# Performance work log

Measured on AMD Instinct MI355X. Metric: run time of the kernel, lower is better.

Reference implementation:

```python
import jax, jax.numpy as jnp
import numpy as np
from jax import lax

DN = ('NCHW', 'OIHW', 'NCHW')

def dsconv(x, dw_w, dw_b, pw_w, pw_b, dilation):
    # depthwise 3x3 (groups = C), padding = dilation, then pointwise 1x1
    C = x.shape[1]
    y = lax.conv_general_dilated(
        x, dw_w, window_strides=(1, 1),
        padding=[(dilation, dilation), (dilation, dilation)],
        rhs_dilation=(dilation, dilation),
        dimension_numbers=DN, feature_group_count=C)
    y = y + dw_b[None, :, None, None]
    y = lax.conv_general_dilated(y, pw_w, window_strides=(1, 1), padding='VALID',
                                 dimension_numbers=DN)
    return y + pw_b[None, :, None, None]


def setup_inputs() -> dict:
    key = jax.random.key(0)
    ks = jax.random.split(key, 16)
    B, C, H, W = 4, 256, 64, 64
    R = C // 8  # reduced_channels = 32
    s = 0.05
    inp = {
        'x': jax.random.normal(ks[0], (B, C, H, W), dtype=jnp.float32),
        # conv1 (dilation 1)
        'c1_dw_w': jax.random.normal(ks[1], (C, 1, 3, 3), dtype=jnp.float32) * s,
        'c1_dw_b': jax.random.normal(ks[2], (C,), dtype=jnp.float32) * s,
        'c1_pw_w': jax.random.normal(ks[3], (R, C, 1, 1), dtype=jnp.float32) * s,
        'c1_pw_b': jax.random.normal(ks[4], (R,), dtype=jnp.float32) * s,
        # conv2 (dilation 3)
        'c2_dw_w': jax.random.normal(ks[5], (C, 1, 3, 3), dtype=jnp.float32) * s,
        'c2_dw_b': jax.random.normal(ks[6], (C,), dtype=jnp.float32) * s,
        'c2_pw_w': jax.random.normal(ks[7], (R, C, 1, 1), dtype=jnp.float32) * s,
        'c2_pw_b': jax.random.normal(ks[8], (R,), dtype=jnp.float32) * s,
        # conv3 (dilation 5)
        'c3_dw_w': jax.random.normal(ks[9], (C, 1, 3, 3), dtype=jnp.float32) * s,
        'c3_dw_b': jax.random.normal(ks[10], (C,), dtype=jnp.float32) * s,
        'c3_pw_w': jax.random.normal(ks[11], (R, C, 1, 1), dtype=jnp.float32) * s,
        'c3_pw_b': jax.random.normal(ks[12], (R,), dtype=jnp.float32) * s,
        # conv_out 1x1: R -> C
        'co_w': jax.random.normal(ks[13], (C, R, 1, 1), dtype=jnp.float32) * s,
        'co_b': jax.random.normal(ks[14], (C,), dtype=jnp.float32) * s,
    }
    return inp


def reference(x, c1_dw_w, c1_dw_b, c1_pw_w, c1_pw_b,
              c2_dw_w, c2_dw_b, c2_pw_w, c2_pw_b,
              c3_dw_w, c3_dw_b, c3_pw_w, c3_pw_b,
              co_w, co_b):
    B, C, H, W = x.shape
    R = C // 8
    N = H * W
    Fp1 = dsconv(x, c1_dw_w, c1_dw_b, c1_pw_w, c1_pw_b, 1).reshape(B, R, N)
    Fp2 = dsconv(x, c2_dw_w, c2_dw_b, c2_pw_w, c2_pw_b, 3).reshape(B, R, N)
    Fp3 = dsconv(x, c3_dw_w, c3_dw_b, c3_pw_w, c3_pw_b, 5).reshape(B, R, N)
    # Mpam[b,i,j] = sum_c Fp2[b,c,i] * Fp3[b,c,j]; softmax over j
    Mpam = jax.nn.softmax(jnp.einsum('bci,bcj->bij', Fp2, Fp3), axis=-1)
    # Fpmap[b,c,i] = sum_j Fp1[b,c,j] * Mpam[i,j]  (matmul with Mpam^T)
    Fpmap = jnp.einsum('bcj,bij->bci', Fp1, Mpam).reshape(B, R, H, W)
    Fpmap = lax.conv_general_dilated(Fpmap, co_w, (1, 1), 'VALID',
                                     dimension_numbers=DN) + co_b[None, :, None, None]
    return x + Fpmap
```

## Files before the change

### kernel.cpp

```cpp
#include <hip/hip_runtime.h>
#include <stdint.h>

#define BB 4
#define CC 256
#define NN 4096
#define RR 32
#define NCHUNK 8
#define JSTEPS (NN / NCHUNK / 32)
#define CSIZE  (NN / NCHUNK)

typedef __attribute__((ext_vector_type(8)))  short  short8;
typedef __attribute__((ext_vector_type(4)))  short  short4v;
typedef __attribute__((ext_vector_type(16))) float  floatx16;

#if defined(__has_builtin)
#if __has_builtin(__builtin_amdgcn_cvt_pk_bf16_f32)
#define HAVE_PK_BF16 1
#endif
#endif

#ifdef HAVE_PK_BF16
typedef __attribute__((ext_vector_type(2))) __bf16 bf16x2;
#endif

static __device__ __forceinline__ unsigned short f2bf_sw(float f) {
    union { float f; unsigned int u; } v; v.f = f;
    unsigned int u = v.u;
    u += 0x7fffu + ((u >> 16) & 1u);
    return (unsigned short)(u >> 16);
}

static __device__ __forceinline__ unsigned int pk_bf16(float a, float b) {
#ifdef HAVE_PK_BF16
    bf16x2 r = __builtin_amdgcn_cvt_pk_bf16_f32(a, b);
    unsigned int u; __builtin_memcpy(&u, &r, 4); return u;
#else
    return (unsigned int)f2bf_sw(a) | ((unsigned int)f2bf_sw(b) << 16);
#endif
}

static __device__ __forceinline__ unsigned short f2bf(float f) {
#ifdef HAVE_PK_BF16
    return (unsigned short)(pk_bf16(f, 0.f) & 0xffffu);
#else
    return f2bf_sw(f);
#endif
}

static __device__ __forceinline__ float bf2f(unsigned short u) {
    union { unsigned int u; float f; } v; v.u = ((unsigned int)u) << 16;
    return v.f;
}

static __device__ __forceinline__ float exp2_fast(float x) {
#if __has_builtin(__builtin_amdgcn_exp2f)
    return __builtin_amdgcn_exp2f(x);
#else
    return exp2f(x);
#endif
}

__global__ __launch_bounds__(256, 4) void k_dw(
    const float* __restrict__ x,
    const float* __restrict__ w1, const float* __restrict__ b1,
    const float* __restrict__ w2, const float* __restrict__ b2,
    const float* __restrict__ w3, const float* __restrict__ b3,
    unsigned short* __restrict__ Dq)
{
    int t = threadIdx.x, lane = t & 63, wv = t >> 6;
    int c = blockIdx.x, b = blockIdx.y;
    int hb = wv * 16;
    const float* xc = x + ((size_t)(b * CC + c)) * NN;
    float row[26];
    #pragma unroll
    for (int k = 0; k < 26; k++) {
        int rr = hb - 5 + k;
        int rc = rr < 0 ? 0 : (rr > 63 ? 63 : rr);
        float v = xc[rc * 64 + lane];
        row[k] = (rr >= 0 && rr <= 63) ? v : 0.f;
    }
    const float* DWW[3] = {w1, w2, w3};
    const float* DWB[3] = {b1, b2, b3};
    #pragma unroll
    for (int p = 0; p < 3; p++) {
        const int d = (p == 0) ? 1 : (p == 1 ? 3 : 5);
        float wt[9];
        #pragma unroll
        for (int q = 0; q < 9; q++) wt[q] = DWW[p][c * 9 + q];
        float bias = DWB[p][c];
        bool okl = lane >= d, okr = lane < 64 - d;
        int lml = okl ? lane - d : 0;
        int lpr = okr ? lane + d : 63;
        float sm[26], sp[26];
        #pragma unroll
        for (int k = 5 - d; k <= 20 + d; k++) {
            float a = __shfl(row[k], lml, 64); sm[k] = okl ? a : 0.f;
            float q2 = __shfl(row[k], lpr, 64); sp[k] = okr ? q2 : 0.f;
        }
        unsigned short* Dp = Dq + (((size_t)p * BB + b) * CC + c) * NN;
        #pragma unroll
        for (int hl = 0; hl < 16; hl++) {
            int k0 = hl + 5 - d, k1 = hl + 5, k2 = hl + 5 + d;
            float o = bias
                + wt[0] * sm[k0] + wt[1] * row[k0] + wt[2] * sp[k0]
                + wt[3] * sm[k1] + wt[4] * row[k1] + wt[5] * sp[k1]
                + wt[6] * sm[k2] + wt[7] * row[k2] + wt[8] * sp[k2];
            Dp[(hb + hl) * 64 + lane] = f2bf(o);
        }
    }
}

__global__ __launch_bounds__(256, 2) void k_pw(
    const unsigned short* __restrict__ Dq,
    const float* __restrict__ p1, const float* __restrict__ pb1,
    const float* __restrict__ p2, const float* __restrict__ pb2,
    const float* __restrict__ p3, const float* __restrict__ pb3,
    unsigned short* __restrict__ V, unsigned short* __restrict__ Qt,
    unsigned short* __restrict__ Kt)
{
    __shared__ unsigned short PW[32 * 264];
    __shared__ unsigned short Dt[128 * 132];
    __shared__ unsigned short Lt[4][32][40];
    int t = threadIdx.x, lane = t & 63, l31 = lane & 31, h = lane >> 5, wv = t >> 6;
    int ntile = blockIdx.x, p = blockIdx.y, b = blockIdx.z;
    const float* pw  = (p == 0) ? p1  : (p == 1 ? p2  : p3);
    const float* pwb = (p == 0) ? pb1 : (p == 1 ? pb2 : pb3);

    {
        int r = t >> 3, cb0 = (t & 7) * 32;
        const float4* src = (const float4*)(pw + r * CC + cb0);
        #pragma unroll
        for (int g = 0; g < 8; g++) {
            float4 f = src[g];
            union { short4v s; unsigned int u[2]; } s4;
            s4.u[0] = pk_bf16(f.x, f.y);
            s4.u[1] = pk_bf16(f.z, f.w);
            *(short4v*)&PW[r * 264 + cb0 + g * 4] = s4.s;
        }
    }
    __syncthreads();

    int n = ntile * 128 + wv * 32 + l31;
    const size_t dbase = ((size_t)p * BB + b) * CC * (size_t)NN;
    int cr = t >> 1, nseg = (t & 1) * 64;
    floatx16 acc = {};

    for (int hc = 0; hc < 2; hc++) {
        const uint4* gsrc = (const uint4*)(Dq + dbase +
                            (size_t)(hc * 128 + cr) * NN + ntile * 128 + nseg);
        uint4 g[8];
        #pragma unroll
        for (int i = 0; i < 8; i++) g[i] = gsrc[i];
        __syncthreads();
        {
            uint2* ldst = (uint2*)&Dt[cr * 132 + nseg];
            #pragma unroll
            for (int i = 0; i < 8; i++) {
                union { uint4 q; uint2 d2[2]; } u; u.q = g[i];
                ldst[2 * i] = u.d2[0];
                ldst[2 * i + 1] = u.d2[1];
            }
        }
        __syncthreads();
        #pragma unroll
        for (int kt = 0; kt < 8; kt++) {
            short8 af = *(const short8*)&PW[l31 * 264 + hc * 128 + kt * 16 + 8 * h];
            short8 bf;
            #pragma unroll
            for (int j = 0; j < 8; j++)
                bf[j] = (short)Dt[(kt * 16 + 8 * h + j) * 132 + wv * 32 + l31];
            acc = __builtin_amdgcn_mfma_f32_32x32x16_bf16(af, bf, acc, 0, 0, 0);
        }
    }

    if (p == 0) {
        #pragma unroll
        for (int rr = 0; rr < 16; rr++) {
            int r = (rr & 3) + 8 * (rr >> 2) + 4 * h;
            V[((size_t)(b * RR + r)) * NN + n] = f2bf(acc[rr] + pwb[r]);
        }
    } else {
        const float sc = (p == 1) ? 1.4426950408889634f : 1.f;
        unsigned short* outp = (p == 1) ? Qt : Kt;
        #pragma unroll
        for (int rr = 0; rr < 16; rr++) {
            int r = (rr & 3) + 8 * (rr >> 2) + 4 * h;
            Lt[wv][l31][r] = f2bf((acc[rr] + pwb[r]) * sc);
        }
        __threadfence_block();
        unsigned short* orow = outp + ((size_t)b * NN + n) * RR + h * 16;
        short8 lo = *(const short8*)&Lt[wv][l31][h * 16];
        *(short8*)orow = lo;
        short8 hi = *(const short8*)&Lt[wv][l31][h * 16 + 8];
        *(short8*)(orow + 8) = hi;
    }
}

__global__ __launch_bounds__(256, 4) void k_attn(
    const unsigned short* __restrict__ Qt, const unsigned short* __restrict__ Kt,
    const unsigned short* __restrict__ V, unsigned short* __restrict__ OPh,
    float* __restrict__ LP)
{
    __shared__ unsigned short Vt[2][32][36];
    int t = threadIdx.x;
    int wave = t >> 6, lane = t & 63, l31 = lane & 31, h = lane >> 5;
    int itile = blockIdx.x * 4 + wave;
    int chunk = blockIdx.y;
    int b = blockIdx.z;
    int i = itile * 32 + l31;

    const short8* qrow = (const short8*)(Qt + ((size_t)b * NN + i) * RR);
    short8 q1 = qrow[h], q2 = qrow[2 + h];

    const unsigned short* Kb = Kt + (size_t)b * NN * RR;
    const unsigned short* Vb = V + (size_t)b * RR * NN;

    int sr = t >> 3, sc = t & 7;
    int scp = (sc & 4) | ((sc & 1) << 1) | ((sc & 2) >> 1);
    const unsigned short* vsrc = Vb + (size_t)sr * NN + chunk * CSIZE + sc * 4;

    floatx16 acc = {};
    float lacc = 0.f;

    *(short4v*)(&Vt[0][sr][scp * 4]) = *(const short4v*)vsrc;
    short4v vnext = *(const short4v*)(vsrc + 32);
    const short8* krow0 = (const short8*)(Kb + (size_t)(chunk * CSIZE + l31) * RR);
    short8 ka1 = krow0[h], ka2 = krow0[2 + h];
    __syncthreads();

    for (int js = 0; js < JSTEPS; js++) {
        int cur = js & 1;
        if (js + 1 < JSTEPS) *(short4v*)(&Vt[1 - cur][sr][scp * 4]) = vnext;
        if (js + 2 < JSTEPS) vnext = *(const short4v*)(vsrc + (js + 2) * 32);

        floatx16 st = {};
        st = __builtin_amdgcn_mfma_f32_32x32x16_bf16(ka1, q1, st, 0, 0, 0);
        st = __builtin_amdgcn_mfma_f32_32x32x16_bf16(ka2, q2, st, 0, 0, 0);
        int jn = (js + 1 < JSTEPS) ? js + 1 : js;
        const short8* krow = (const short8*)(Kb + (size_t)(chunk * CSIZE + jn * 32 + l31) * RR);
        ka1 = krow[h]; ka2 = krow[2 + h];

        float p[16];
        #pragma unroll
        for (int r = 0; r < 16; r++) { p[r] = exp2_fast(st[r]); lacc += p[r]; }
        union { short8 s; unsigned int u[4]; } pa1, pa2;
        #pragma unroll
        for (int r = 0; r < 8; r += 2) {
            pa1.u[r >> 1] = pk_bf16(p[r], p[r + 1]);
            pa2.u[r >> 1] = pk_bf16(p[r + 8], p[r + 9]);
        }
        const unsigned short* vrow = &Vt[cur][l31][0];
        short8 vb1 = *(const short8*)(vrow + 8 * h);
        short8 vb2 = *(const short8*)(vrow + 16 + 8 * h);
        acc = __builtin_amdgcn_mfma_f32_32x32x16_bf16(pa1.s, vb1, acc, 0, 0, 0);
        acc = __builtin_amdgcn_mfma_f32_32x32x16_bf16(pa2.s, vb2, acc, 0, 0, 0);
        __syncthreads();
    }
    size_t slot = ((size_t)(b * 128 + itile) * NCHUNK + chunk) * 64 + lane;
    unsigned short* op = OPh + slot * 16;
    union { short8 s; unsigned int u[4]; } o1, o2;
    #pragma unroll
    for (int r = 0; r < 8; r += 2) {
        o1.u[r >> 1] = pk_bf16(acc[r], acc[r + 1]);
        o2.u[r >> 1] = pk_bf16(acc[r + 8], acc[r + 9]);
    }
    *(short8*)op = o1.s;
    *(short8*)(op + 8) = o2.s;
    LP[slot] = lacc;
}

__global__ __launch_bounds__(256, 4) void k_out(
    const float* __restrict__ x, const unsigned short* __restrict__ OPh,
    const float* __restrict__ LP, const float* __restrict__ cw,
    const float* __restrict__ cb, float* __restrict__ out)
{
    __shared__ float linv[32];
    __shared__ unsigned short Ft[32][36];
    __shared__ unsigned short CW[256 * 36];
    int t = threadIdx.x, lane = t & 63, l31 = lane & 31, h = lane >> 5, wv = t >> 6;
    int itile = blockIdx.x, b = blockIdx.y;
    size_t base = (size_t)(b * 128 + itile) * NCHUNK;

    {
        const float4* src = (const float4*)(cw + (size_t)t * RR);
        #pragma unroll
        for (int g = 0; g < 8; g++) {
            float4 f = src[g];
            union { short4v s; unsigned int u[2]; } s4;
            s4.u[0] = pk_bf16(f.x, f.y);
            s4.u[1] = pk_bf16(f.z, f.w);
            *(short4v*)&CW[t * 36 + g * 4] = s4.s;
        }
    }
    int g = wv;
    float s0 = 0.f, s1 = 0.f, s2 = 0.f, s3 = 0.f;
    #pragma unroll
    for (int ch = 0; ch < NCHUNK; ch++) {
        short4v v = *(const short4v*)(OPh + ((base + ch) * 64 + lane) * 16 + 4 * g);
        s0 += bf2f((unsigned short)v[0]); s1 += bf2f((unsigned short)v[1]);
        s2 += bf2f((unsigned short)v[2]); s3 += bf2f((unsigned short)v[3]);
    }
    if (t < 32) {
        float sl = 0.f;
        #pragma unroll
        for (int ch = 0; ch < NCHUNK; ch++) {
            sl += LP[(base + ch) * 64 + t] + LP[(base + ch) * 64 + t + 32];
        }
        linv[t] = 1.f / sl;
    }
    __syncthreads();
    {
        float sv[4] = {s0, s1, s2, s3};
        #pragma unroll
        for (int j = 0; j < 4; j++) {
            int reg = 4 * g + j;
            int il = (reg & 3) + 8 * (reg >> 2) + 4 * h;
            Ft[il][l31] = f2bf(sv[j] * linv[il]);
        }
    }
    __syncthreads();
    #pragma unroll
    for (int cti = 0; cti < 2; cti++) {
        int co0 = (wv * 2 + cti) * 32;
        const unsigned short* arow = &CW[(co0 + l31) * 36 + 8 * h];
        union { short8 s; short4v hh[2]; } a1, a2, b1, b2;
        a1.hh[0] = *(const short4v*)arow;
        a1.hh[1] = *(const short4v*)(arow + 4);
        a2.hh[0] = *(const short4v*)(arow + 16);
        a2.hh[1] = *(const short4v*)(arow + 20);
        const unsigned short* brow = &Ft[l31][8 * h];
        b1.hh[0] = *(const short4v*)brow;
        b1.hh[1] = *(const short4v*)(brow + 4);
        b2.hh[0] = *(const short4v*)(brow + 16);
        b2.hh[1] = *(const short4v*)(brow + 20);
        floatx16 acc = {};
        acc = __builtin_amdgcn_mfma_f32_32x32x16_bf16(a1.s, b1.s, acc, 0, 0, 0);
        acc = __builtin_amdgcn_mfma_f32_32x32x16_bf16(a2.s, b2.s, acc, 0, 0, 0);
        #pragma unroll
        for (int rr = 0; rr < 16; rr++) {
            int co = co0 + (rr & 3) + 8 * (rr >> 2) + 4 * h;
            size_t o = ((size_t)(b * CC + co)) * NN + itile * 32 + l31;
            out[o] = x[o] + acc[rr] + cb[co];
        }
    }
}

extern "C" void kernel_launch(void* const* d_in, const int* in_sizes, int n_in,
                              void* d_out, int out_size, void* d_ws, size_t ws_size,
                              hipStream_t stream) {
    const float* x = (const float*)d_in[0];
    char* ws = (char*)d_ws;
    unsigned short* Dq  = (unsigned short*)(ws);
    unsigned short* OPh = (unsigned short*)(ws);
    unsigned short* Qt  = (unsigned short*)(ws + 25165824);
    unsigned short* Kt  = (unsigned short*)(ws + 26214400);
    unsigned short* V   = (unsigned short*)(ws + 27262976);
    float*          LP  = (float*)(ws + 28311552);

    hipLaunchKernelGGL(k_dw, dim3(CC, BB), dim3(256), 0, stream, x,
                       (const float*)d_in[1], (const float*)d_in[2],
                       (const float*)d_in[5], (const float*)d_in[6],
                       (const float*)d_in[9], (const float*)d_in[10], Dq);
    hipLaunchKernelGGL(k_pw, dim3(32, 3, BB), dim3(256), 0, stream, Dq,
                       (const float*)d_in[3], (const float*)d_in[4],
                       (const float*)d_in[7], (const float*)d_in[8],
                       (const float*)d_in[11], (const float*)d_in[12],
                       V, Qt, Kt);
    hipLaunchKernelGGL(k_attn, dim3(32, NCHUNK, BB), dim3(256), 0, stream,
                       Qt, Kt, V, OPh, LP);
    hipLaunchKernelGGL(k_out, dim3(128, BB), dim3(256), 0, stream,
                       x, OPh, LP, (const float*)d_in[13], (const float*)d_in[14],
                       (float*)d_out);
}
```

Before: 140.0 us.

## Process two query tiles per wave in attention kernel to reuse K/V

Each wave in k_attn now handles two 32-row query tiles (itA and itB = itA+64) against the same K fragment and the same V tile in shared memory, and the grid x-dimension is halved to match. This halves K global loads, V shared-memory staging and block synchronisations per unit of work, and gives two independent MFMA chains that can interleave. The costs are roughly doubled accumulator register use (launch bounds drop from 4 to 2 blocks per SM) and half as many blocks (512), which lowers occupancy and latency hiding.

```diff
diff --git a/kernel.cpp b/kernel.cpp
--- a/kernel.cpp
+++ b/kernel.cpp
@@ -196,7 +196,7 @@
     }
 }
 
-__global__ __launch_bounds__(256, 4) void k_attn(
+__global__ __launch_bounds__(256, 2) void k_attn(
     const unsigned short* __restrict__ Qt, const unsigned short* __restrict__ Kt,
     const unsigned short* __restrict__ V, unsigned short* __restrict__ OPh,
     float* __restrict__ LP)
@@ -204,13 +204,17 @@
     __shared__ unsigned short Vt[2][32][36];
     int t = threadIdx.x;
     int wave = t >> 6, lane = t & 63, l31 = lane & 31, h = lane >> 5;
-    int itile = blockIdx.x * 4 + wave;
+    int itA = blockIdx.x * 4 + wave;
+    int itB = itA + 64;
     int chunk = blockIdx.y;
     int b = blockIdx.z;
-    int i = itile * 32 + l31;
-
-    const short8* qrow = (const short8*)(Qt + ((size_t)b * NN + i) * RR);
-    short8 q1 = qrow[h], q2 = qrow[2 + h];
+    int iA = itA * 32 + l31;
+    int iB = itB * 32 + l31;
+
+    const short8* qrA = (const short8*)(Qt + ((size_t)b * NN + iA) * RR);
+    short8 qa1 = qrA[h], qa2 = qrA[2 + h];
+    const short8* qrB = (const short8*)(Qt + ((size_t)b * NN + iB) * RR);
+    short8 qb1 = qrB[h], qb2 = qrB[2 + h];
 
     const unsigned short* Kb = Kt + (size_t)b * NN * RR;
     const unsigned short* Vb = V + (size_t)b * RR * NN;
@@ -219,8 +223,8 @@
     int scp = (sc & 4) | ((sc & 1) << 1) | ((sc & 2) >> 1);
     const unsigned short* vsrc = Vb + (size_t)sr * NN + chunk * CSIZE + sc * 4;
 
-    floatx16 acc = {};
-    float lacc = 0.f;
+    floatx16 accA = {}, accB = {};
+    float laccA = 0.f, laccB = 0.f;
 
     *(short4v*)(&Vt[0][sr][scp * 4]) = *(const short4v*)vsrc;
     short4v vnext = *(const short4v*)(vsrc + 32);
@@ -233,40 +237,75 @@
         if (js + 1 < JSTEPS) *(short4v*)(&Vt[1 - cur][sr][scp * 4]) = vnext;
         if (js + 2 < JSTEPS) vnext = *(const short4v*)(vsrc + (js + 2) * 32);
 
-        floatx16 st = {};
-        st = __builtin_amdgcn_mfma_f32_32x32x16_bf16(ka1, q1, st, 0, 0, 0);
-        st = __builtin_amdgcn_mfma_f32_32x32x16_bf16(ka2, q2, st, 0, 0, 0);
-        int jn = (js + 1 < JSTEPS) ? js + 1 : js;
-        const short8* krow = (const short8*)(Kb + (size_t)(chunk * CSIZE + jn * 32 + l31) * RR);
-        ka1 = krow[h]; ka2 = krow[2 + h];
-
-        float p[16];
-        #pragma unroll
-        for (int r = 0; r < 16; r++) { p[r] = exp2_fast(st[r]); lacc += p[r]; }
-        union { short8 s; unsigned int u[4]; } pa1, pa2;
-        #pragma unroll
-        for (int r = 0; r < 8; r += 2) {
-            pa1.u[r >> 1] = pk_bf16(p[r], p[r + 1]);
-            pa2.u[r >> 1] = pk_bf16(p[r + 8], p[r + 9]);
-        }
         const unsigned short* vrow = &Vt[cur][l31][0];
         short8 vb1 = *(const short8*)(vrow + 8 * h);
         short8 vb2 = *(const short8*)(vrow + 16 + 8 * h);
-        acc = __builtin_amdgcn_mfma_f32_32x32x16_bf16(pa1.s, vb1, acc, 0, 0, 0);
-        acc = __builtin_amdgcn_mfma_f32_32x32x16_bf16(pa2.s, vb2, acc, 0, 0, 0);
+
+        {
+            floatx16 st = {};
+            st = __builtin_amdgcn_mfma_f32_32x32x16_bf16(ka1, qa1, st, 0, 0, 0);
+            st = __builtin_amdgcn_mfma_f32_32x32x16_bf16(ka2, qa2, st, 0, 0, 0);
+            float p[16];
+            #pragma unroll
+            for (int r = 0; r < 16; r++) { p[r] = exp2_fast(st[r]); laccA += p[r]; }
+            union { short8 s; unsigned int u[4]; } pa1, pa2;
+            #pragma unroll
+            for (int r = 0; r < 8; r += 2) {
+                pa1.u[r >> 1] = pk_bf16(p[r], p[r + 1]);
+                pa2.u[r >> 1] = pk_bf16(p[r + 8], p[r + 9]);
+            }
+            accA = __builtin_amdgcn_mfma_f32_32x32x16_bf16(pa1.s, vb1, accA, 0, 0, 0);
+            accA = __builtin_amdgcn_mfma_f32_32x32x16_bf16(pa2.s, vb2, accA, 0, 0, 0);
+        }
+
+        {
+            floatx16 st = {};
+            st = __builtin_amdgcn_mfma_f32_32x32x16_bf16(ka1, qb1, st, 0, 0, 0);
+            st = __builtin_amdgcn_mfma_f32_32x32x16_bf16(ka2, qb2, st, 0, 0, 0);
+            int jn = (js + 1 < JSTEPS) ? js + 1 : js;
+            const short8* krow = (const short8*)(Kb + (size_t)(chunk * CSIZE + jn * 32 + l31) * RR);
+            ka1 = krow[h]; ka2 = krow[2 + h];
+            float p[16];
+            #pragma unroll
+            for (int r = 0; r < 16; r++) { p[r] = exp2_fast(st[r]); laccB += p[r]; }
+            union { short8 s; unsigned int u[4]; } pa1, pa2;
+            #pragma unroll
+            for (int r = 0; r < 8; r += 2) {
+                pa1.u[r >> 1] = pk_bf16(p[r], p[r + 1]);
+                pa2.u[r >> 1] = pk_bf16(p[r + 8], p[r + 9]);
+            }
+            accB = __builtin_amdgcn_mfma_f32_32x32x16_bf16(pa1.s, vb1, accB, 0, 0, 0);
+            accB = __builtin_amdgcn_mfma_f32_32x32x16_bf16(pa2.s, vb2, accB, 0, 0, 0);
+        }
         __syncthreads();
     }
-    size_t slot = ((size_t)(b * 128 + itile) * NCHUNK + chunk) * 64 + lane;
-    unsigned short* op = OPh + slot * 16;
-    union { short8 s; unsigned int u[4]; } o1, o2;
-    #pragma unroll
-    for (int r = 0; r < 8; r += 2) {
-        o1.u[r >> 1] = pk_bf16(acc[r], acc[r + 1]);
-        o2.u[r >> 1] = pk_bf16(acc[r + 8], acc[r + 9]);
-    }
-    *(short8*)op = o1.s;
-    *(short8*)(op + 8) = o2.s;
-    LP[slot] = lacc;
+
+    {
+        size_t slot = ((size_t)(b * 128 + itA) * NCHUNK + chunk) * 64 + lane;
+        unsigned short* op = OPh + slot * 16;
+        union { short8 s; unsigned int u[4]; } o1, o2;
+        #pragma unroll
+        for (int r = 0; r < 8; r += 2) {
+            o1.u[r >> 1] = pk_bf16(accA[r], accA[r + 1]);
+            o2.u[r >> 1] = pk_bf16(accA[r + 8], accA[r + 9]);
+        }
+        *(short8*)op = o1.s;
+        *(short8*)(op + 8) = o2.s;
+        LP[slot] = laccA;
+    }
+    {
+        size_t slot = ((size_t)(b * 128 + itB) * NCHUNK + chunk) * 64 + lane;
+        unsigned short* op = OPh + slot * 16;
+        union { short8 s; unsigned int u[4]; } o1, o2;
+        #pragma unroll
+        for (int r = 0; r < 8; r += 2) {
+            o1.u[r >> 1] = pk_bf16(accB[r], accB[r + 1]);
+            o2.u[r >> 1] = pk_bf16(accB[r + 8], accB[r + 9]);
+        }
+        *(short8*)op = o1.s;
+        *(short8*)(op + 8) = o2.s;
+        LP[slot] = laccB;
+    }
 }
 
 __global__ __launch_bounds__(256, 4) void k_out(
@@ -366,7 +405,7 @@
                        (const float*)d_in[7], (const float*)d_in[8],
                        (const float*)d_in[11], (const float*)d_in[12],
                        V, Qt, Kt);
-    hipLaunchKernelGGL(k_attn, dim3(32, NCHUNK, BB), dim3(256), 0, stream,
+    hipLaunchKernelGGL(k_attn, dim3(16, NCHUNK, BB), dim3(256), 0, stream,
                        Qt, Kt, V, OPh, LP);
     hipLaunchKernelGGL(k_out, dim3(128, BB), dim3(256), 0, stream,
                        x, OPh, LP, (const float*)d_in[13], (const float*)d_in[14],
```

After: 139.8 us. Within noise of the previous version (-0.2%).
